# Kernel tuning notes

Hardware: AMD Instinct MI355X
Metric: run time of the kernel (lower is better)

## Reference

```python
import jax, jax.numpy as jnp
import numpy as np


def _cheby_stack(xt, degree):
    # Note: this layer uses T1 = 2*tanh(x) (non-standard), recurrence T_n = 2*xt*T_{n-1} - T_{n-2}
    Ts = [jnp.ones_like(xt)]
    if degree > 0:
        Ts.append(2.0 * xt)
    for n in range(2, degree + 1):
        Ts.append(2.0 * xt * Ts[-1] - Ts[-2])
    return jnp.stack(Ts, axis=2)  # (b, p, n)


def _kan_layer(x, W, tW):
    deg = tW.shape[-1] - 1
    cheby = _cheby_stack(jnp.tanh(x), deg)  # (b, p, n)
    # Fused form of einsum('bpn,qpn->bqp') then einsum('bqp,qp->bq');
    # XLA contracts (tW*W) first, avoiding the huge (b,q,p) intermediate.
    return jnp.einsum('bpn,qpn,qp->bq', cheby, tW, W)


def _cheby_gelu(x, degree=5):
    # Here T1 = tanh(x) (standard), then GeLU(exact) of stacked basis, summed.
    xt = jnp.tanh(x)
    Ts = [jnp.ones_like(xt), xt]
    for n in range(2, degree + 1):
        Ts.append(2.0 * xt * Ts[-1] - Ts[-2])
    st = jnp.stack(Ts, axis=-1)
    return jax.nn.gelu(st, approximate=False).sum(axis=-1)


def setup_inputs() -> dict:
    key = jax.random.key(0)
    ks = jax.random.split(key, 12)
    batch, in_dim, mid, out_dim, deg = 131072, 8, 128, 1, 8
    nfeat = 32
    d = {}
    d['x'] = jax.random.normal(ks[0], (batch, in_dim), jnp.float32)
    d['B'] = jax.random.normal(ks[1], (in_dim, nfeat), jnp.float32)  # scale=1.0
    dims = [(mid, 2 * nfeat), (mid, mid), (mid, mid), (mid, mid), (out_dim, mid)]
    for i, (q, p) in enumerate(dims):
        std_W = np.sqrt(5.0 / (p + q)).astype(np.float32)
        std_tW = np.float32(1.0 / (deg + 1))
        d[f'W{i}'] = std_W * jax.random.normal(ks[2 + 2 * i], (q, p), jnp.float32)
        d[f'tW{i}'] = 0.1 + std_tW * jax.random.normal(ks[3 + 2 * i], (q, p, deg + 1), jnp.float32)
    return d


def reference(x, B, W0, tW0, W1, tW1, W2, tW2, W3, tW3, W4, tW4):
    # FourierFeatures
    proj = (2.0 * jnp.pi) * (x @ B)
    h = jnp.concatenate([jnp.sin(proj), jnp.cos(proj)], axis=-1)  # (b, 64)
    # KAN layers; dropout_prob=0.0 (eval) -> identity. Middle layers get residual
    h = _kan_layer(h, W0, tW0)
    h = _kan_layer(h, W1, tW1) + h
    h = _kan_layer(h, W2, tW2) + h
    h = _kan_layer(h, W3, tW3) + h
    h = _kan_layer(h, W4, tW4)  # (b, 1)
    return _cheby_gelu(h, degree=5)
```

## Files before the change

kernel.cpp:

```cpp
#include <hip/hip_runtime.h>

#define TPB 256

typedef _Float16 f16x8 __attribute__((ext_vector_type(8)));
typedef __fp16 h16x2 __attribute__((ext_vector_type(2)));
typedef float f32x4 __attribute__((ext_vector_type(4)));

static constexpr int WT_L0 = 0;
static constexpr int WT_L1 = 65536;
static constexpr int WT_L2 = 196608;
static constexpr int WT_L3 = 327680;
static constexpr int WT_END = 458752;
static constexpr int F32_BASE = WT_END;
static constexpr int MST = 132;

__device__ __forceinline__ float fast_tanh2(float x) {
  float e = __expf(2.0f * x);
  return fmaf(-4.0f, __builtin_amdgcn_rcpf(e + 1.0f), 2.0f);
}
__device__ __forceinline__ float gelu_exact(float v) {
  return 0.5f * v * (1.0f + erff(v * 0.70710678f));
}

__global__ void fuse_w_f16(const float* __restrict__ W, const float* __restrict__ tW,
                           _Float16* __restrict__ out_hi, _Float16* __restrict__ out_lo,
                           int P, int total, int sbits) {
  int i = blockIdx.x * 256 + threadIdx.x;
  if (i >= total) return;
  int j = i & 7, q = (i >> 3) & 15, g = (i >> 7) & 3, t = (i >> 9) & 7;
  int s = (i >> 12) & ((1 << sbits) - 1);
  int n1 = i >> (12 + sbits);
  int p = s * 32 + g * 8 + j;
  int qg = t * 16 + q;
  float v = tW[(qg * P + p) * 9 + (n1 + 1)] * W[qg * P + p];
  _Float16 hi = (_Float16)v;
  out_hi[i] = hi;
  out_lo[i] = (_Float16)(v - (float)hi);
}
__global__ void fuse_bias(const float* __restrict__ W, const float* __restrict__ tW,
                          float* __restrict__ bias, int P, int Q) {
  int q = blockIdx.x * 64 + threadIdx.x;
  if (q >= Q) return;
  float s = 0.0f;
  for (int p = 0; p < P; ++p) s += tW[(q * P + p) * 9] * W[q * P + p];
  bias[q] = s;
}
__global__ void fuse_w4(const float* __restrict__ W, const float* __restrict__ tW,
                        float* __restrict__ out) {
  int i = blockIdx.x * 128 + threadIdx.x;
  if (i >= 1152) return;
  out[i] = tW[i] * W[i / 9];
}

template <int S, bool RES>
__device__ __forceinline__ void layer_mfma(const float* __restrict__ mlds,
                                           const _Float16* __restrict__ wt_hi,
                                           const _Float16* __restrict__ wt_lo,
                                           const float* __restrict__ bias,
                                           f32x4 (&acc)[2][8], int l) {
#pragma unroll
  for (int qt = 0; qt < 8; ++qt) {
    float bv = bias[qt * 16 + (l & 15)];
#pragma unroll
    for (int mt = 0; mt < 2; ++mt)
#pragma unroll
      for (int j = 0; j < 4; ++j) {
        if (RES) acc[mt][qt][j] += bv; else acc[mt][qt][j] = bv;
      }
  }
  const _Float16* wl_hi = wt_hi + (size_t)l * 8;
  const _Float16* wl_lo = wt_lo + (size_t)l * 8;
#pragma unroll 1
  for (int s = 0; s < S; ++s) {
    float mv[2][8], up[2][8], uc[2][8];
#pragma unroll
    for (int mt = 0; mt < 2; ++mt) {
      const f32x4* mp =
          (const f32x4*)(mlds + (mt * 16 + (l & 15)) * MST + s * 32 + ((l >> 4) * 8));
      f32x4 lo = mp[0], hi = mp[1];
#pragma unroll
      for (int i = 0; i < 4; ++i) { mv[mt][i] = lo[i]; mv[mt][4 + i] = hi[i]; }
#pragma unroll
      for (int i = 0; i < 8; ++i) { up[mt][i] = 1.0f; uc[mt][i] = mv[mt][i]; }
    }
#pragma unroll 1
    for (int n = 1; n <= 8; ++n) {
      const size_t toff = (size_t)((n - 1) * S + s) * 8 * 512;
      const _Float16* wn_hi = wl_hi + toff;
      const _Float16* wn_lo = wl_lo + toff;
      f16x8 bh[8], bl[8];
#pragma unroll
      for (int t = 0; t < 8; ++t) bh[t] = *(const f16x8*)(wn_hi + t * 512);
#pragma unroll
      for (int t = 0; t < 8; ++t) bl[t] = *(const f16x8*)(wn_lo + t * 512);
      f16x8 af_hi[2], af_lo[2];
#pragma unroll
      for (int mt = 0; mt < 2; ++mt) {
        union U8 { h16x2 h2[4]; f16x8 v; } uh, ul;
#pragma unroll
        for (int i = 0; i < 4; ++i) {
          float v0 = uc[mt][2 * i], v1 = uc[mt][2 * i + 1];
          h16x2 h = __builtin_amdgcn_cvt_pkrtz(v0, v1);
          float l0 = v0 - (float)h[0];
          float l1 = v1 - (float)h[1];
          uh.h2[i] = h;
          ul.h2[i] = __builtin_amdgcn_cvt_pkrtz(l0, l1);
        }
        af_hi[mt] = uh.v;
        af_lo[mt] = ul.v;
      }
#pragma unroll
      for (int mt = 0; mt < 2; ++mt)
#pragma unroll
        for (int i = 0; i < 8; ++i) {
          float u = fmaf(mv[mt][i], uc[mt][i], -up[mt][i]);
          up[mt][i] = uc[mt][i];
          uc[mt][i] = u;
        }
#pragma unroll
      for (int t = 0; t < 8; ++t) {
        acc[0][t] = __builtin_amdgcn_mfma_f32_16x16x32_f16(af_hi[0], bh[t], acc[0][t], 0, 0, 0);
        acc[1][t] = __builtin_amdgcn_mfma_f32_16x16x32_f16(af_hi[1], bh[t], acc[1][t], 0, 0, 0);
      }
#pragma unroll
      for (int t = 0; t < 8; ++t) {
        acc[0][t] = __builtin_amdgcn_mfma_f32_16x16x32_f16(af_lo[0], bh[t], acc[0][t], 0, 0, 0);
        acc[1][t] = __builtin_amdgcn_mfma_f32_16x16x32_f16(af_lo[1], bh[t], acc[1][t], 0, 0, 0);
      }
#pragma unroll
      for (int t = 0; t < 8; ++t) {
        acc[0][t] = __builtin_amdgcn_mfma_f32_16x16x32_f16(af_hi[0], bl[t], acc[0][t], 0, 0, 0);
        acc[1][t] = __builtin_amdgcn_mfma_f32_16x16x32_f16(af_hi[1], bl[t], acc[1][t], 0, 0, 0);
      }
    }
  }
}

__device__ __forceinline__ void write_m(float* __restrict__ mlds,
                                        const f32x4 (&acc)[2][8], int l) {
#pragma unroll
  for (int mt = 0; mt < 2; ++mt)
#pragma unroll
    for (int qt = 0; qt < 8; ++qt)
#pragma unroll
      for (int j = 0; j < 4; ++j) {
        int row = mt * 16 + ((l >> 4) * 4 + j);
        mlds[row * MST + qt * 16 + (l & 15)] = fast_tanh2(acc[mt][qt][j]);
      }
}

__global__ void __launch_bounds__(TPB, 2)
kan_mfma(const float* __restrict__ x, const float* __restrict__ Bm,
         const _Float16* __restrict__ wt_hi, const _Float16* __restrict__ wt_lo,
         const float* __restrict__ bias, const float* __restrict__ w4,
         float* __restrict__ out) {
  __shared__ float mlds_all[4][32 * MST];
  int tid = threadIdx.x;
  int l = tid & 63;
  int w = tid >> 6;
  float* mlds = mlds_all[w];
  int row0 = blockIdx.x * 128 + w * 32;

  {
    int r = l & 31, hh = l >> 5;
    const float4* xp = (const float4*)(x + (size_t)(row0 + r) * 8);
    float4 a = xp[0], c4 = xp[1];
    float xv[8] = {a.x, a.y, a.z, a.w, c4.x, c4.y, c4.z, c4.w};
#pragma unroll
    for (int jj = 0; jj < 16; ++jj) {
      int j = hh * 16 + jj;
      float pr = 0.0f;
#pragma unroll
      for (int k = 0; k < 8; ++k) pr = fmaf(xv[k], Bm[k * 32 + j], pr);
      float ang = 6.2831853071795864f * pr;
      float sv, cv;
      sincosf(ang, &sv, &cv);
      mlds[r * MST + j] = fast_tanh2(sv);
      mlds[r * MST + 32 + j] = fast_tanh2(cv);
    }
  }

  f32x4 acc[2][8];
  layer_mfma<2, false>(mlds, wt_hi + WT_L0, wt_lo + WT_L0, bias + 0, acc, l);
  write_m(mlds, acc, l);
  layer_mfma<4, true>(mlds, wt_hi + WT_L1, wt_lo + WT_L1, bias + 128, acc, l);
  write_m(mlds, acc, l);
  layer_mfma<4, true>(mlds, wt_hi + WT_L2, wt_lo + WT_L2, bias + 256, acc, l);
  write_m(mlds, acc, l);
  layer_mfma<4, true>(mlds, wt_hi + WT_L3, wt_lo + WT_L3, bias + 384, acc, l);
  write_m(mlds, acc, l);

  {
    int r = l & 31, ph = l >> 5;
    const float* mrow = mlds + r * MST + ph * 64;
    const float* w4h = w4 + ph * 64 * 9;
    float part = 0.0f;
#pragma unroll 4
    for (int p = 0; p < 64; ++p) {
      float mm = mrow[p];
      const float* wp = w4h + p * 9;
      part += wp[0];
      part = fmaf(mm, wp[1], part);
      float u2 = 1.0f, u1 = mm;
#pragma unroll
      for (int n = 2; n < 9; ++n) {
        float u = fmaf(mm, u1, -u2);
        u2 = u1;
        u1 = u;
        part = fmaf(u, wp[n], part);
      }
    }
    part += __shfl_xor(part, 32);
    if (l < 32) {
      float v = part;
      float t = 0.5f * fast_tanh2(v);
      float m2 = t + t;
      float tm2 = 1.0f, tm1 = t;
      float y = gelu_exact(1.0f) + gelu_exact(t);
#pragma unroll
      for (int n = 2; n <= 5; ++n) {
        float tn = fmaf(m2, tm1, -tm2);
        tm2 = tm1;
        tm1 = tn;
        y += gelu_exact(tn);
      }
      out[row0 + r] = y;
    }
  }
}

extern "C" void kernel_launch(void* const* d_in, const int* in_sizes, int n_in,
                              void* d_out, int out_size, void* d_ws, size_t ws_size,
                              hipStream_t stream) {
  const float* x   = (const float*)d_in[0];
  const float* Bm  = (const float*)d_in[1];
  const float* W0  = (const float*)d_in[2];
  const float* tW0 = (const float*)d_in[3];
  const float* W1  = (const float*)d_in[4];
  const float* tW1 = (const float*)d_in[5];
  const float* W2  = (const float*)d_in[6];
  const float* tW2 = (const float*)d_in[7];
  const float* W3  = (const float*)d_in[8];
  const float* tW3 = (const float*)d_in[9];
  const float* W4  = (const float*)d_in[10];
  const float* tW4 = (const float*)d_in[11];

  _Float16* wt_hi = (_Float16*)d_ws;
  _Float16* wt_lo = wt_hi + WT_END;
  float* fws = (float*)d_ws + F32_BASE;
  float* bias = fws;
  float* w4 = fws + 512;

  fuse_w_f16<<<65536 / 256, 256, 0, stream>>>(W0, tW0, wt_hi + WT_L0, wt_lo + WT_L0, 64, 65536, 1);
  fuse_w_f16<<<131072 / 256, 256, 0, stream>>>(W1, tW1, wt_hi + WT_L1, wt_lo + WT_L1, 128, 131072, 2);
  fuse_w_f16<<<131072 / 256, 256, 0, stream>>>(W2, tW2, wt_hi + WT_L2, wt_lo + WT_L2, 128, 131072, 2);
  fuse_w_f16<<<131072 / 256, 256, 0, stream>>>(W3, tW3, wt_hi + WT_L3, wt_lo + WT_L3, 128, 131072, 2);
  fuse_bias<<<2, 64, 0, stream>>>(W0, tW0, bias + 0, 64, 128);
  fuse_bias<<<2, 64, 0, stream>>>(W1, tW1, bias + 128, 128, 128);
  fuse_bias<<<2, 64, 0, stream>>>(W2, tW2, bias + 256, 128, 128);
  fuse_bias<<<2, 64, 0, stream>>>(W3, tW3, bias + 384, 128, 128);
  fuse_w4<<<9, 128, 0, stream>>>(W4, tW4, w4);

  kan_mfma<<<131072 / 128, TPB, 0, stream>>>(x, Bm, wt_hi, wt_lo, bias, w4, (float*)d_out);
}
```

Measured before the change: 388.1 us.

## Split each block's rows across a 2x2 wave grid sharing one LDS tile

Previously each wave handled 32 rows independently across all 128 output columns with a private LDS tile. Now a block handles 64 rows, and its four waves form a 2x2 grid over rows and output-column halves. Each wave loads only half of the weight tiles per k-step, and its accumulator shrinks from 2x8 to 2x4, which should cut register use so that launch bounds can go to 3 blocks per CU. The cost is block-wide __syncthreads between layers, recurrence recomputation duplicated across the two column waves, twice as many blocks, and s_setprio hints around the MFMA bursts.

```diff
diff --git a/kernel.cpp b/kernel.cpp
--- a/kernel.cpp
+++ b/kernel.cpp
@@ -53,152 +53,166 @@
 }
 
 template <int S, bool RES>
-__device__ __forceinline__ void layer_mfma(const float* __restrict__ mlds,
-                                           const _Float16* __restrict__ wt_hi,
-                                           const _Float16* __restrict__ wt_lo,
-                                           const float* __restrict__ bias,
-                                           f32x4 (&acc)[2][8], int l) {
-#pragma unroll
-  for (int qt = 0; qt < 8; ++qt) {
-    float bv = bias[qt * 16 + (l & 15)];
-#pragma unroll
-    for (int mt = 0; mt < 2; ++mt)
+__device__ __forceinline__ void layer22(const float* __restrict__ mT,
+                                        const _Float16* __restrict__ wt_hi,
+                                        const _Float16* __restrict__ wt_lo,
+                                        const float* __restrict__ biasL,
+                                        f32x4 (&acc)[2][4], int l, int wr, int wc) {
+  const int c15 = l & 15, g = l >> 4;
+#pragma unroll
+  for (int qt = 0; qt < 4; ++qt) {
+    float bv = biasL[wc * 64 + qt * 16 + c15];
+#pragma unroll
+    for (int rtl = 0; rtl < 2; ++rtl)
 #pragma unroll
       for (int j = 0; j < 4; ++j) {
-        if (RES) acc[mt][qt][j] += bv; else acc[mt][qt][j] = bv;
-      }
-  }
-  const _Float16* wl_hi = wt_hi + (size_t)l * 8;
-  const _Float16* wl_lo = wt_lo + (size_t)l * 8;
+        if (RES) acc[rtl][qt][j] += bv; else acc[rtl][qt][j] = bv;
+      }
+  }
+  const _Float16* bh_base = wt_hi + wc * 2048 + l * 8;
+  const _Float16* bl_base = wt_lo + wc * 2048 + l * 8;
+  float mv[2][8], up[2][8], uc[2][8];
 #pragma unroll 1
-  for (int s = 0; s < S; ++s) {
-    float mv[2][8], up[2][8], uc[2][8];
-#pragma unroll
-    for (int mt = 0; mt < 2; ++mt) {
-      const f32x4* mp =
-          (const f32x4*)(mlds + (mt * 16 + (l & 15)) * MST + s * 32 + ((l >> 4) * 8));
-      f32x4 lo = mp[0], hi = mp[1];
-#pragma unroll
-      for (int i = 0; i < 4; ++i) { mv[mt][i] = lo[i]; mv[mt][4 + i] = hi[i]; }
-#pragma unroll
-      for (int i = 0; i < 8; ++i) { up[mt][i] = 1.0f; uc[mt][i] = mv[mt][i]; }
-    }
-#pragma unroll 1
-    for (int n = 1; n <= 8; ++n) {
-      const size_t toff = (size_t)((n - 1) * S + s) * 8 * 512;
-      const _Float16* wn_hi = wl_hi + toff;
-      const _Float16* wn_lo = wl_lo + toff;
-      f16x8 bh[8], bl[8];
-#pragma unroll
-      for (int t = 0; t < 8; ++t) bh[t] = *(const f16x8*)(wn_hi + t * 512);
-#pragma unroll
-      for (int t = 0; t < 8; ++t) bl[t] = *(const f16x8*)(wn_lo + t * 512);
-      f16x8 af_hi[2], af_lo[2];
-#pragma unroll
-      for (int mt = 0; mt < 2; ++mt) {
-        union U8 { h16x2 h2[4]; f16x8 v; } uh, ul;
-#pragma unroll
-        for (int i = 0; i < 4; ++i) {
-          float v0 = uc[mt][2 * i], v1 = uc[mt][2 * i + 1];
-          h16x2 h = __builtin_amdgcn_cvt_pkrtz(v0, v1);
-          float l0 = v0 - (float)h[0];
-          float l1 = v1 - (float)h[1];
-          uh.h2[i] = h;
-          ul.h2[i] = __builtin_amdgcn_cvt_pkrtz(l0, l1);
+  for (int k = 0; k < 8 * S; ++k) {
+    int s = k >> 3, n1 = k & 7;
+    size_t toff = (size_t)(n1 * S + s) * 4096;
+    f16x8 bh[4], bl[4];
+#pragma unroll
+    for (int qt = 0; qt < 4; ++qt) {
+      bh[qt] = *(const f16x8*)(bh_base + toff + qt * 512);
+      bl[qt] = *(const f16x8*)(bl_base + toff + qt * 512);
+    }
+    if (n1 == 0) {
+#pragma unroll
+      for (int rtl = 0; rtl < 2; ++rtl) {
+        const f32x4* mp = (const f32x4*)(mT + (wr * 32 + rtl * 16 + c15) * MST +
+                                         s * 32 + g * 8);
+        f32x4 a = mp[0], b = mp[1];
+#pragma unroll
+        for (int i = 0; i < 4; ++i) { mv[rtl][i] = a[i]; mv[rtl][4 + i] = b[i]; }
+#pragma unroll
+        for (int i = 0; i < 8; ++i) { up[rtl][i] = 1.0f; uc[rtl][i] = mv[rtl][i]; }
+      }
+    } else {
+#pragma unroll
+      for (int rtl = 0; rtl < 2; ++rtl)
+#pragma unroll
+        for (int i = 0; i < 8; ++i) {
+          float u = fmaf(mv[rtl][i], uc[rtl][i], -up[rtl][i]);
+          up[rtl][i] = uc[rtl][i];
+          uc[rtl][i] = u;
         }
-        af_hi[mt] = uh.v;
-        af_lo[mt] = ul.v;
-      }
-#pragma unroll
-      for (int mt = 0; mt < 2; ++mt)
-#pragma unroll
-        for (int i = 0; i < 8; ++i) {
-          float u = fmaf(mv[mt][i], uc[mt][i], -up[mt][i]);
-          up[mt][i] = uc[mt][i];
-          uc[mt][i] = u;
-        }
-#pragma unroll
-      for (int t = 0; t < 8; ++t) {
-        acc[0][t] = __builtin_amdgcn_mfma_f32_16x16x32_f16(af_hi[0], bh[t], acc[0][t], 0, 0, 0);
-        acc[1][t] = __builtin_amdgcn_mfma_f32_16x16x32_f16(af_hi[1], bh[t], acc[1][t], 0, 0, 0);
-      }
-#pragma unroll
-      for (int t = 0; t < 8; ++t) {
-        acc[0][t] = __builtin_amdgcn_mfma_f32_16x16x32_f16(af_lo[0], bh[t], acc[0][t], 0, 0, 0);
-        acc[1][t] = __builtin_amdgcn_mfma_f32_16x16x32_f16(af_lo[1], bh[t], acc[1][t], 0, 0, 0);
-      }
-#pragma unroll
-      for (int t = 0; t < 8; ++t) {
-        acc[0][t] = __builtin_amdgcn_mfma_f32_16x16x32_f16(af_hi[0], bl[t], acc[0][t], 0, 0, 0);
-        acc[1][t] = __builtin_amdgcn_mfma_f32_16x16x32_f16(af_hi[1], bl[t], acc[1][t], 0, 0, 0);
-      }
-    }
-  }
-}
-
-__device__ __forceinline__ void write_m(float* __restrict__ mlds,
-                                        const f32x4 (&acc)[2][8], int l) {
-#pragma unroll
-  for (int mt = 0; mt < 2; ++mt)
-#pragma unroll
-    for (int qt = 0; qt < 8; ++qt)
+    }
+    f16x8 afh[2], afl[2];
+#pragma unroll
+    for (int rtl = 0; rtl < 2; ++rtl) {
+      union UU { h16x2 h2[4]; f16x8 v; } uh, ul;
+#pragma unroll
+      for (int ii = 0; ii < 4; ++ii) {
+        float v0 = uc[rtl][2 * ii], v1 = uc[rtl][2 * ii + 1];
+        h16x2 h = __builtin_amdgcn_cvt_pkrtz(v0, v1);
+        uh.h2[ii] = h;
+        ul.h2[ii] = __builtin_amdgcn_cvt_pkrtz(v0 - (float)h[0], v1 - (float)h[1]);
+      }
+      afh[rtl] = uh.v;
+      afl[rtl] = ul.v;
+    }
+    __builtin_amdgcn_s_setprio(1);
+#pragma unroll
+    for (int qt = 0; qt < 4; ++qt)
+#pragma unroll
+      for (int rtl = 0; rtl < 2; ++rtl)
+        acc[rtl][qt] = __builtin_amdgcn_mfma_f32_16x16x32_f16(afh[rtl], bh[qt],
+                                                              acc[rtl][qt], 0, 0, 0);
+#pragma unroll
+    for (int qt = 0; qt < 4; ++qt)
+#pragma unroll
+      for (int rtl = 0; rtl < 2; ++rtl)
+        acc[rtl][qt] = __builtin_amdgcn_mfma_f32_16x16x32_f16(afl[rtl], bh[qt],
+                                                              acc[rtl][qt], 0, 0, 0);
+#pragma unroll
+    for (int qt = 0; qt < 4; ++qt)
+#pragma unroll
+      for (int rtl = 0; rtl < 2; ++rtl)
+        acc[rtl][qt] = __builtin_amdgcn_mfma_f32_16x16x32_f16(afh[rtl], bl[qt],
+                                                              acc[rtl][qt], 0, 0, 0);
+    __builtin_amdgcn_s_setprio(0);
+  }
+}
+
+__device__ __forceinline__ void write_m(float* __restrict__ mT,
+                                        const f32x4 (&acc)[2][4], int l, int wr, int wc) {
+  const int c15 = l & 15, g = l >> 4;
+#pragma unroll
+  for (int rtl = 0; rtl < 2; ++rtl)
+#pragma unroll
+    for (int qt = 0; qt < 4; ++qt)
 #pragma unroll
       for (int j = 0; j < 4; ++j) {
-        int row = mt * 16 + ((l >> 4) * 4 + j);
-        mlds[row * MST + qt * 16 + (l & 15)] = fast_tanh2(acc[mt][qt][j]);
-      }
-}
-
-__global__ void __launch_bounds__(TPB, 2)
+        int row = wr * 32 + rtl * 16 + g * 4 + j;
+        int col = wc * 64 + qt * 16 + c15;
+        mT[row * MST + col] = fast_tanh2(acc[rtl][qt][j]);
+      }
+}
+
+__global__ void __launch_bounds__(TPB, 3)
 kan_mfma(const float* __restrict__ x, const float* __restrict__ Bm,
          const _Float16* __restrict__ wt_hi, const _Float16* __restrict__ wt_lo,
          const float* __restrict__ bias, const float* __restrict__ w4,
          float* __restrict__ out) {
-  __shared__ float mlds_all[4][32 * MST];
+  __shared__ float mT[64 * MST];
   int tid = threadIdx.x;
   int l = tid & 63;
   int w = tid >> 6;
-  float* mlds = mlds_all[w];
-  int row0 = blockIdx.x * 128 + w * 32;
+  int wr = w >> 1, wc = w & 1;
+  int row0 = blockIdx.x * 64;
 
   {
-    int r = l & 31, hh = l >> 5;
-    const float4* xp = (const float4*)(x + (size_t)(row0 + r) * 8);
+    const float4* xp = (const float4*)(x + (size_t)(row0 + l) * 8);
     float4 a = xp[0], c4 = xp[1];
     float xv[8] = {a.x, a.y, a.z, a.w, c4.x, c4.y, c4.z, c4.w};
 #pragma unroll
-    for (int jj = 0; jj < 16; ++jj) {
-      int j = hh * 16 + jj;
+    for (int jj = 0; jj < 8; ++jj) {
+      int j = w * 8 + jj;
       float pr = 0.0f;
 #pragma unroll
       for (int k = 0; k < 8; ++k) pr = fmaf(xv[k], Bm[k * 32 + j], pr);
       float ang = 6.2831853071795864f * pr;
       float sv, cv;
       sincosf(ang, &sv, &cv);
-      mlds[r * MST + j] = fast_tanh2(sv);
-      mlds[r * MST + 32 + j] = fast_tanh2(cv);
-    }
-  }
-
-  f32x4 acc[2][8];
-  layer_mfma<2, false>(mlds, wt_hi + WT_L0, wt_lo + WT_L0, bias + 0, acc, l);
-  write_m(mlds, acc, l);
-  layer_mfma<4, true>(mlds, wt_hi + WT_L1, wt_lo + WT_L1, bias + 128, acc, l);
-  write_m(mlds, acc, l);
-  layer_mfma<4, true>(mlds, wt_hi + WT_L2, wt_lo + WT_L2, bias + 256, acc, l);
-  write_m(mlds, acc, l);
-  layer_mfma<4, true>(mlds, wt_hi + WT_L3, wt_lo + WT_L3, bias + 384, acc, l);
-  write_m(mlds, acc, l);
+      mT[l * MST + j] = fast_tanh2(sv);
+      mT[l * MST + 32 + j] = fast_tanh2(cv);
+    }
+  }
+  __syncthreads();
+
+  f32x4 acc[2][4];
+  layer22<2, false>(mT, wt_hi + WT_L0, wt_lo + WT_L0, bias + 0, acc, l, wr, wc);
+  __syncthreads();
+  write_m(mT, acc, l, wr, wc);
+  __syncthreads();
+  layer22<4, true>(mT, wt_hi + WT_L1, wt_lo + WT_L1, bias + 128, acc, l, wr, wc);
+  __syncthreads();
+  write_m(mT, acc, l, wr, wc);
+  __syncthreads();
+  layer22<4, true>(mT, wt_hi + WT_L2, wt_lo + WT_L2, bias + 256, acc, l, wr, wc);
+  __syncthreads();
+  write_m(mT, acc, l, wr, wc);
+  __syncthreads();
+  layer22<4, true>(mT, wt_hi + WT_L3, wt_lo + WT_L3, bias + 384, acc, l, wr, wc);
+  __syncthreads();
+  write_m(mT, acc, l, wr, wc);
+  __syncthreads();
 
   {
-    int r = l & 31, ph = l >> 5;
-    const float* mrow = mlds + r * MST + ph * 64;
-    const float* w4h = w4 + ph * 64 * 9;
+    int r16 = l & 15, pq = l >> 4;
+    int r = w * 16 + r16;
+    const float* w4h = w4 + pq * 32 * 9;
     float part = 0.0f;
 #pragma unroll 4
-    for (int p = 0; p < 64; ++p) {
-      float mm = mrow[p];
-      const float* wp = w4h + p * 9;
+    for (int pp = 0; pp < 32; ++pp) {
+      float mm = mT[r * MST + pq * 32 + pp];
+      const float* wp = w4h + pp * 9;
       part += wp[0];
       part = fmaf(mm, wp[1], part);
       float u2 = 1.0f, u1 = mm;
@@ -210,8 +224,9 @@
         part = fmaf(u, wp[n], part);
       }
     }
+    part += __shfl_xor(part, 16);
     part += __shfl_xor(part, 32);
-    if (l < 32) {
+    if (l < 16) {
       float v = part;
       float t = 0.5f * fast_tanh2(v);
       float m2 = t + t;
@@ -261,5 +276,5 @@
   fuse_bias<<<2, 64, 0, stream>>>(W3, tW3, bias + 384, 128, 128);
   fuse_w4<<<9, 128, 0, stream>>>(W4, tW4, w4);
 
-  kan_mfma<<<131072 / 128, TPB, 0, stream>>>(x, Bm, wt_hi, wt_lo, bias, w4, (float*)d_out);
-}
+  kan_mfma<<<131072 / 64, TPB, 0, stream>>>(x, Bm, wt_hi, wt_lo, bias, w4, (float*)d_out);
+}
```

Result: slower. 435.7 us (+12.3%).
